# Kernel optimization log

Measured on AMD Instinct MI355X. Metric: run time of the kernel, lower is better.

## Reference

```python
import jax, jax.numpy as jnp
import numpy as np


def setup_inputs() -> dict:
    key = jax.random.key(0)
    k1, k2, k3, k4, k5 = jax.random.split(key, 5)
    B, T, U, D = 4, 256, 64, 512
    H, V = 512, 1024  # forward_output_size, num_classes
    return {
        "encoder_outputs": jax.random.normal(k1, (B, T, D), dtype=jnp.float32),
        "decoder_outputs": jax.random.normal(k2, (B, U, D), dtype=jnp.float32),
        "w1": jax.random.normal(k3, (H, 2 * D), dtype=jnp.float32) * 0.02,
        "b1": jax.random.normal(k4, (H,), dtype=jnp.float32) * 0.02,
        "w2": jax.random.normal(k5, (V, H), dtype=jnp.float32) * 0.02,
    }


def reference(encoder_outputs, decoder_outputs, w1, b1, w2):
    # Faithful to: concat([enc broadcast to (B,T,U,D), dec broadcast to (B,T,U,D)], -1)
    # -> Linear(w1,b1) -> GELU(tanh) -> Linear(w2, no bias).
    # Linear on the concat equals split-weight projections summed via broadcast
    # (classic RNNT joint decomposition): same math, avoids the (B,T,U,2D) tensor.
    D = encoder_outputs.shape[-1]
    w_enc, w_dec = w1[:, :D], w1[:, D:]
    enc_proj = jnp.einsum("btd,hd->bth", encoder_outputs, w_enc)  # (B,T,H)
    dec_proj = jnp.einsum("bud,hd->buh", decoder_outputs, w_dec)  # (B,U,H)
    hidden = enc_proj[:, :, None, :] + dec_proj[:, None, :, :] + b1  # (B,T,U,H)
    hidden = jax.nn.gelu(hidden, approximate=True)  # tanh approximation, matches nn.GELU('tanh')
    logits = jnp.einsum("btuh,vh->btuv", hidden, w2)  # (B,T,U,V)
    return logits
```

## Files before the change

### kernel.cpp

```cpp
#include <hip/hip_runtime.h>
#include <hip/hip_bf16.h>
#include <stdint.h>


typedef __bf16 bf16_t;
typedef bf16_t bf16x8 __attribute__((ext_vector_type(8)));
typedef float f32x4 __attribute__((ext_vector_type(4)));

#define GLD16(gp, lp)                                                          \
  __builtin_amdgcn_global_load_lds(                                            \
      (const __attribute__((address_space(1))) void*)(gp),                     \
      (__attribute__((address_space(3))) void*)(lp), 16, 0, 0)

__device__ __forceinline__ unsigned short f2bf(float f) {
  unsigned int u = __float_as_uint(f);
  unsigned int r = (u + 0x7FFFu + ((u >> 16) & 1u)) >> 16;
  return (unsigned short)r;
}

__device__ __forceinline__ float gelu_f(float x) {
  float t = tanhf(0.7978845608028654f * x + 0.035677408136300125f * (x * x * x));
  return 0.5f * x * (1.0f + t);
}

__global__ __launch_bounds__(256) void prep_kernel(
    const float* __restrict__ enc, const float* __restrict__ dec,
    const float* __restrict__ w1, const float* __restrict__ w2,
    unsigned short* __restrict__ o) {
  int i = (blockIdx.x * 256 + threadIdx.x) * 4;
  float4 v;
  if (i < 524288) {
    v = *(const float4*)(enc + i);
  } else if (i < 655360) {
    v = *(const float4*)(dec + (i - 524288));
  } else if (i < 917504) {
    int j = i - 655360;
    v = *(const float4*)(w1 + (j >> 9) * 1024 + (j & 511));
  } else if (i < 1179648) {
    int j = i - 917504;
    v = *(const float4*)(w1 + (j >> 9) * 1024 + 512 + (j & 511));
  } else {
    v = *(const float4*)(w2 + (i - 1179648));
  }
  ushort4 r;
  r.x = f2bf(v.x); r.y = f2bf(v.y); r.z = f2bf(v.z); r.w = f2bf(v.w);
  *(ushort4*)(o + i) = r;
}

__global__ __launch_bounds__(256) void hidden_kernel(
    const float* __restrict__ ep, const float* __restrict__ dp,
    const float* __restrict__ b1, unsigned short* __restrict__ o) {
  int g = blockIdx.x * 256 + threadIdx.x;
  int m = g >> 7;
  int h = (g & 127) << 2;
  int er = m >> 6;
  int dr = ((m >> 14) << 6) | (m & 63);
  float4 e = *(const float4*)(ep + er * 512 + h);
  float4 d = *(const float4*)(dp + dr * 512 + h);
  float4 b = *(const float4*)(b1 + h);
  ushort4 r;
  r.x = f2bf(gelu_f(e.x + d.x + b.x));
  r.y = f2bf(gelu_f(e.y + d.y + b.y));
  r.z = f2bf(gelu_f(e.z + d.z + b.z));
  r.w = f2bf(gelu_f(e.w + d.w + b.w));
  *(ushort4*)(o + (size_t)g * 4) = r;
}

__global__ __launch_bounds__(256) void gemm_bt(
    const bf16_t* __restrict__ A, const bf16_t* __restrict__ B,
    float* __restrict__ C, int M, int N, int K) {
  __shared__ bf16_t sA[128 * 32];
  __shared__ bf16_t sB[128 * 32];

  const int tid = threadIdx.x;
  const int lane = tid & 63;
  const int w = tid >> 6;
  const int m0 = blockIdx.y * 128;
  const int n0 = blockIdx.x * 128;
  const int wm = (w >> 1) * 64;
  const int wn = (w & 1) * 64;

  const int colS = (lane & 3) * 8;
  const int rA0 = (w * 2 + 0) * 16 + (lane >> 2);
  const int rA1 = (w * 2 + 1) * 16 + (lane >> 2);
  const bf16_t* gA0 = A + (size_t)(m0 + rA0) * K + colS;
  const bf16_t* gA1 = A + (size_t)(m0 + rA1) * K + colS;
  const bf16_t* gB0 = B + (size_t)(n0 + rA0) * K + colS;
  const bf16_t* gB1 = B + (size_t)(n0 + rA1) * K + colS;
  bf16_t* lA0 = sA + (w * 2 + 0) * 512;
  bf16_t* lA1 = sA + (w * 2 + 1) * 512;
  bf16_t* lB0 = sB + (w * 2 + 0) * 512;
  bf16_t* lB1 = sB + (w * 2 + 1) * 512;

  const int offA = ((wm + (lane & 15)) * 32 + (lane >> 4) * 8) >> 3;
  const int offB = ((wn + (lane & 15)) * 32 + (lane >> 4) * 8) >> 3;
  const bf16x8* pA = (const bf16x8*)sA;
  const bf16x8* pB = (const bf16x8*)sB;

  f32x4 acc[4][4] = {};

  for (int kt = 0; kt < K; kt += 32) {
    GLD16(gA0 + kt, lA0);
    GLD16(gA1 + kt, lA1);
    GLD16(gB0 + kt, lB0);
    GLD16(gB1 + kt, lB1);
    __syncthreads();

    bf16x8 af[4], bb[4];
#pragma unroll
    for (int i = 0; i < 4; i++) af[i] = pA[offA + i * 64];
#pragma unroll
    for (int j = 0; j < 4; j++) bb[j] = pB[offB + j * 64];
#pragma unroll
    for (int i = 0; i < 4; i++)
#pragma unroll
      for (int j = 0; j < 4; j++)
        acc[i][j] = __builtin_amdgcn_mfma_f32_16x16x32_bf16(af[i], bb[j],
                                                            acc[i][j], 0, 0, 0);
    __syncthreads();
  }

  const int crow = m0 + wm + (lane >> 4) * 4;
  const int ccol = n0 + wn + (lane & 15);
  float* Cp = C + (size_t)crow * N + ccol;
#pragma unroll
  for (int i = 0; i < 4; i++)
#pragma unroll
    for (int r = 0; r < 4; r++)
#pragma unroll
      for (int j = 0; j < 4; j++)
        Cp[(size_t)(i * 16 + r) * N + j * 16] = acc[i][j][r];
}

extern "C" void kernel_launch(void* const* d_in, const int* in_sizes, int n_in,
                              void* d_out, int out_size, void* d_ws,
                              size_t ws_size, hipStream_t stream) {
  const float* enc = (const float*)d_in[0];
  const float* dec = (const float*)d_in[1];
  const float* w1  = (const float*)d_in[2];
  const float* b1  = (const float*)d_in[3];
  const float* w2  = (const float*)d_in[4];
  float* out = (float*)d_out;

  unsigned short* bf      = (unsigned short*)d_ws;
  unsigned short* ws_enc  = bf;
  unsigned short* ws_dec  = bf + 524288;
  unsigned short* ws_wenc = bf + 655360;
  unsigned short* ws_wdec = bf + 917504;
  unsigned short* ws_w2   = bf + 1179648;
  float* encp = (float*)((char*)d_ws + 3407872);
  float* decp = encp + 524288;
  unsigned short* hid = (unsigned short*)(decp + 131072);

  prep_kernel<<<1664, 256, 0, stream>>>(enc, dec, w1, w2, bf);

  gemm_bt<<<dim3(4, 8), 256, 0, stream>>>((const bf16_t*)ws_enc,
                                          (const bf16_t*)ws_wenc, encp,
                                          1024, 512, 512);
  gemm_bt<<<dim3(4, 2), 256, 0, stream>>>((const bf16_t*)ws_dec,
                                          (const bf16_t*)ws_wdec, decp,
                                          256, 512, 512);

  hidden_kernel<<<32768, 256, 0, stream>>>(encp, decp, b1, hid);

  gemm_bt<<<dim3(8, 512), 256, 0, stream>>>((const bf16_t*)hid,
                                            (const bf16_t*)ws_w2, out,
                                            65536, 1024, 512);
}
```

Before: 412.6 us.

## Deepen GEMM K-tile with XOR-swizzled LDS, merge projections, cheaper GELU

The GEMM core now stages 64-wide K tiles instead of 32, halving the number of barriers per K sweep. It uses an XOR swizzle on LDS columns so fragment reads avoid bank conflicts. The two projection GEMMs are merged into one launch. The hidden kernel processes 8 elements per thread, and GELU-tanh is rewritten as x*sigmoid(2u) using fast exp and rcp. The fast GELU is slightly less accurate, and the larger LDS tiles may lower occupancy.

```diff
diff --git a/kernel.cpp b/kernel.cpp
--- a/kernel.cpp
+++ b/kernel.cpp
@@ -6,6 +6,7 @@
 typedef __bf16 bf16_t;
 typedef bf16_t bf16x8 __attribute__((ext_vector_type(8)));
 typedef float f32x4 __attribute__((ext_vector_type(4)));
+typedef unsigned short u16x8 __attribute__((ext_vector_type(8)));
 
 #define GLD16(gp, lp)                                                          \
   __builtin_amdgcn_global_load_lds(                                            \
@@ -14,13 +15,13 @@
 
 __device__ __forceinline__ unsigned short f2bf(float f) {
   unsigned int u = __float_as_uint(f);
-  unsigned int r = (u + 0x7FFFu + ((u >> 16) & 1u)) >> 16;
-  return (unsigned short)r;
+  return (unsigned short)((u + 0x7FFFu + ((u >> 16) & 1u)) >> 16);
 }
 
 __device__ __forceinline__ float gelu_f(float x) {
-  float t = tanhf(0.7978845608028654f * x + 0.035677408136300125f * (x * x * x));
-  return 0.5f * x * (1.0f + t);
+  float t = 1.5957691216057308f * x + 0.07135481283867141f * (x * x * x);
+  float e = __expf(-t);
+  return x * __builtin_amdgcn_rcpf(1.0f + e);
 }
 
 __global__ __launch_bounds__(256) void prep_kernel(
@@ -51,72 +52,76 @@
     const float* __restrict__ ep, const float* __restrict__ dp,
     const float* __restrict__ b1, unsigned short* __restrict__ o) {
   int g = blockIdx.x * 256 + threadIdx.x;
-  int m = g >> 7;
-  int h = (g & 127) << 2;
+  int m = g >> 6;
+  int h = (g & 63) << 3;
   int er = m >> 6;
   int dr = ((m >> 14) << 6) | (m & 63);
-  float4 e = *(const float4*)(ep + er * 512 + h);
-  float4 d = *(const float4*)(dp + dr * 512 + h);
-  float4 b = *(const float4*)(b1 + h);
-  ushort4 r;
-  r.x = f2bf(gelu_f(e.x + d.x + b.x));
-  r.y = f2bf(gelu_f(e.y + d.y + b.y));
-  r.z = f2bf(gelu_f(e.z + d.z + b.z));
-  r.w = f2bf(gelu_f(e.w + d.w + b.w));
-  *(ushort4*)(o + (size_t)g * 4) = r;
+  float4 e0 = *(const float4*)(ep + er * 512 + h);
+  float4 e1 = *(const float4*)(ep + er * 512 + h + 4);
+  float4 d0 = *(const float4*)(dp + dr * 512 + h);
+  float4 d1 = *(const float4*)(dp + dr * 512 + h + 4);
+  float4 b0 = *(const float4*)(b1 + h);
+  float4 b1v = *(const float4*)(b1 + h + 4);
+  u16x8 r;
+  r[0] = f2bf(gelu_f(e0.x + d0.x + b0.x));
+  r[1] = f2bf(gelu_f(e0.y + d0.y + b0.y));
+  r[2] = f2bf(gelu_f(e0.z + d0.z + b0.z));
+  r[3] = f2bf(gelu_f(e0.w + d0.w + b0.w));
+  r[4] = f2bf(gelu_f(e1.x + d1.x + b1v.x));
+  r[5] = f2bf(gelu_f(e1.y + d1.y + b1v.y));
+  r[6] = f2bf(gelu_f(e1.z + d1.z + b1v.z));
+  r[7] = f2bf(gelu_f(e1.w + d1.w + b1v.w));
+  *(u16x8*)(o + (size_t)g * 8) = r;
 }
 
-__global__ __launch_bounds__(256) void gemm_bt(
+__device__ __forceinline__ void gemm_core(
     const bf16_t* __restrict__ A, const bf16_t* __restrict__ B,
-    float* __restrict__ C, int M, int N, int K) {
-  __shared__ bf16_t sA[128 * 32];
-  __shared__ bf16_t sB[128 * 32];
+    float* __restrict__ C, int m0, int n0, int N, int K) {
+  __shared__ bf16_t sA[128 * 64];
+  __shared__ bf16_t sB[128 * 64];
 
   const int tid = threadIdx.x;
   const int lane = tid & 63;
   const int w = tid >> 6;
-  const int m0 = blockIdx.y * 128;
-  const int n0 = blockIdx.x * 128;
   const int wm = (w >> 1) * 64;
   const int wn = (w & 1) * 64;
 
-  const int colS = (lane & 3) * 8;
-  const int rA0 = (w * 2 + 0) * 16 + (lane >> 2);
-  const int rA1 = (w * 2 + 1) * 16 + (lane >> 2);
-  const bf16_t* gA0 = A + (size_t)(m0 + rA0) * K + colS;
-  const bf16_t* gA1 = A + (size_t)(m0 + rA1) * K + colS;
-  const bf16_t* gB0 = B + (size_t)(n0 + rA0) * K + colS;
-  const bf16_t* gB1 = B + (size_t)(n0 + rA1) * K + colS;
-  bf16_t* lA0 = sA + (w * 2 + 0) * 512;
-  bf16_t* lA1 = sA + (w * 2 + 1) * 512;
-  bf16_t* lB0 = sB + (w * 2 + 0) * 512;
-  bf16_t* lB1 = sB + (w * 2 + 1) * 512;
+  const int srow = w * 32 + (lane >> 3);
+  const int scol = (((lane & 7) ^ (lane >> 3)) << 3);
+  const bf16_t* gA = A + (size_t)(m0 + srow) * K + scol;
+  const bf16_t* gB = B + (size_t)(n0 + srow) * K + scol;
 
-  const int offA = ((wm + (lane & 15)) * 32 + (lane >> 4) * 8) >> 3;
-  const int offB = ((wn + (lane & 15)) * 32 + (lane >> 4) * 8) >> 3;
+  const int rowA = wm + (lane & 15);
+  const int rowB = wn + (lane & 15);
+  const int sw0 = (lane >> 4) ^ (lane & 7);
   const bf16x8* pA = (const bf16x8*)sA;
   const bf16x8* pB = (const bf16x8*)sB;
 
   f32x4 acc[4][4] = {};
 
-  for (int kt = 0; kt < K; kt += 32) {
-    GLD16(gA0 + kt, lA0);
-    GLD16(gA1 + kt, lA1);
-    GLD16(gB0 + kt, lB0);
-    GLD16(gB1 + kt, lB1);
+  for (int kt = 0; kt < K; kt += 64) {
+#pragma unroll
+    for (int j = 0; j < 4; j++) {
+      GLD16(gA + (size_t)(j * 8) * K + kt, sA + (w * 4 + j) * 512);
+      GLD16(gB + (size_t)(j * 8) * K + kt, sB + (w * 4 + j) * 512);
+    }
     __syncthreads();
 
-    bf16x8 af[4], bb[4];
 #pragma unroll
-    for (int i = 0; i < 4; i++) af[i] = pA[offA + i * 64];
+    for (int kk = 0; kk < 2; kk++) {
+      const int sw = sw0 ^ (kk << 2);
+      bf16x8 af[4], bb[4];
 #pragma unroll
-    for (int j = 0; j < 4; j++) bb[j] = pB[offB + j * 64];
+      for (int i = 0; i < 4; i++) af[i] = pA[(rowA + i * 16) * 8 + sw];
 #pragma unroll
-    for (int i = 0; i < 4; i++)
+      for (int j = 0; j < 4; j++) bb[j] = pB[(rowB + j * 16) * 8 + sw];
 #pragma unroll
-      for (int j = 0; j < 4; j++)
-        acc[i][j] = __builtin_amdgcn_mfma_f32_16x16x32_bf16(af[i], bb[j],
-                                                            acc[i][j], 0, 0, 0);
+      for (int i = 0; i < 4; i++)
+#pragma unroll
+        for (int j = 0; j < 4; j++)
+          acc[i][j] = __builtin_amdgcn_mfma_f32_16x16x32_bf16(
+              af[i], bb[j], acc[i][j], 0, 0, 0);
+    }
     __syncthreads();
   }
 
@@ -130,6 +135,24 @@
 #pragma unroll
       for (int j = 0; j < 4; j++)
         Cp[(size_t)(i * 16 + r) * N + j * 16] = acc[i][j][r];
+}
+
+__global__ __launch_bounds__(256) void gemm_big(
+    const bf16_t* __restrict__ A, const bf16_t* __restrict__ B,
+    float* __restrict__ C, int M, int N, int K) {
+  gemm_core(A, B, C, blockIdx.y * 128, blockIdx.x * 128, N, K);
+}
+
+__global__ __launch_bounds__(256) void proj_kernel(
+    const bf16_t* __restrict__ encA, const bf16_t* __restrict__ wenc,
+    float* __restrict__ encC, const bf16_t* __restrict__ decA,
+    const bf16_t* __restrict__ wdec, float* __restrict__ decC) {
+  int by = blockIdx.y;
+  if (by < 8) {
+    gemm_core(encA, wenc, encC, by * 128, blockIdx.x * 128, 512, 512);
+  } else {
+    gemm_core(decA, wdec, decC, (by - 8) * 128, blockIdx.x * 128, 512, 512);
+  }
 }
 
 extern "C" void kernel_launch(void* const* d_in, const int* in_sizes, int n_in,
@@ -154,16 +177,12 @@
 
   prep_kernel<<<1664, 256, 0, stream>>>(enc, dec, w1, w2, bf);
 
-  gemm_bt<<<dim3(4, 8), 256, 0, stream>>>((const bf16_t*)ws_enc,
-                                          (const bf16_t*)ws_wenc, encp,
-                                          1024, 512, 512);
-  gemm_bt<<<dim3(4, 2), 256, 0, stream>>>((const bf16_t*)ws_dec,
-                                          (const bf16_t*)ws_wdec, decp,
-                                          256, 512, 512);
+  proj_kernel<<<dim3(4, 10), 256, 0, stream>>>(
+      (const bf16_t*)ws_enc, (const bf16_t*)ws_wenc, encp,
+      (const bf16_t*)ws_dec, (const bf16_t*)ws_wdec, decp);
 
-  hidden_kernel<<<32768, 256, 0, stream>>>(encp, decp, b1, hid);
+  hidden_kernel<<<16384, 256, 0, stream>>>(encp, decp, b1, hid);
 
-  gemm_bt<<<dim3(8, 512), 256, 0, stream>>>((const bf16_t*)hid,
-                                            (const bf16_t*)ws_w2, out,
-                                            65536, 1024, 512);
+  gemm_big<<<dim3(8, 512), 256, 0, stream>>>(
+      (const bf16_t*)hid, (const bf16_t*)ws_w2, out, 65536, 1024, 512);
 }
```

Result: faster. 384.0 us (-6.9%).
